# Kernel optimization log

Measured on AMD Instinct MI355X. Metric: run time of the kernel, lower is better.

The kernel has to match this reference:

```python
import jax, jax.numpy as jnp
import numpy as np

H, C = 8, 16          # heads, per-head dim; hidden = H*C = 128
NEG_SLOPE = 0.2       # GATConv default
EPS = 1e-5            # GraphNorm eps


def setup_inputs() -> dict:
    key = jax.random.key(0)
    ks = iter(jax.random.split(key, 64))
    Np, Na, D, E = 100000, 50000, 128, 500000
    s = 1.0 / np.sqrt(D)

    def w(shape, scale=1.0):
        return jax.random.normal(next(ks), shape, jnp.float32) * scale

    inp = {
        'x_paper': w((Np, D)),
        'x_author': w((Na, D)),
        'edge_writes': jnp.stack([
            jax.random.randint(next(ks), (E,), 0, Na),
            jax.random.randint(next(ks), (E,), 0, Np)]).astype(jnp.int32),
        'edge_cites': jnp.stack([
            jax.random.randint(next(ks), (E,), 0, Np),
            jax.random.randint(next(ks), (E,), 0, Np)]).astype(jnp.int32),
        'W_lin_paper': w((D, 128), s), 'b_lin_paper': jnp.zeros((128,), jnp.float32),
        'W_lin_author': w((D, 128), s), 'b_lin_author': jnp.zeros((128,), jnp.float32),
        'Wsrc_writes': w((128, 128), s), 'Wdst_writes': w((128, 128), s),
        'atts_writes': w((H, C), 0.1), 'attd_writes': w((H, C), 0.1),
        'bias_writes': jnp.zeros((128,), jnp.float32),
        'Wsrc_cites': w((128, 128), s), 'Wdst_cites': w((128, 128), s),
        'atts_cites': w((H, C), 0.1), 'attd_cites': w((H, C), 0.1),
        'bias_cites': jnp.zeros((128,), jnp.float32),
        'gnw_paper': jnp.ones((128,), jnp.float32), 'gnb_paper': jnp.zeros((128,), jnp.float32),
        'gnm_paper': jnp.ones((128,), jnp.float32),
        'gnw_author': jnp.ones((128,), jnp.float32), 'gnb_author': jnp.zeros((128,), jnp.float32),
        'gnm_author': jnp.ones((128,), jnp.float32),
        'W2_paper': w((128, 128), s), 'b2_paper': jnp.zeros((128,), jnp.float32),
        'W2_author': w((128, 128), s), 'b2_author': jnp.zeros((128,), jnp.float32),
    }
    return inp


def _gat(src_emb, dst_emb, ei, Wsrc, Wdst, att_s, att_d, bias, n_dst):
    # PyG GATConv, bipartite input, concat=True, add_self_loops=True (eval / no dropout)
    n_self = min(src_emb.shape[0], n_dst)
    loops = jnp.arange(n_self, dtype=ei.dtype)
    src = jnp.concatenate([ei[0], loops])
    dst = jnp.concatenate([ei[1], loops])
    xs = (src_emb @ Wsrc).reshape(-1, H, C)          # [Ns,H,C]
    xd = (dst_emb @ Wdst).reshape(-1, H, C)          # [Nd,H,C]
    a_s = (xs * att_s).sum(-1)                       # [Ns,H]
    a_d = (xd * att_d).sum(-1)                       # [Nd,H]
    e = jax.nn.leaky_relu(a_s[src] + a_d[dst], NEG_SLOPE)   # [E,H]
    m = jax.ops.segment_max(e, dst, num_segments=n_dst)
    m = jnp.where(jnp.isfinite(m), m, 0.0)           # guard empty segments
    p = jnp.exp(e - m[dst])
    denom = jax.ops.segment_sum(p, dst, num_segments=n_dst)
    alpha = p / (denom[dst] + 1e-16)                 # segment softmax over dst
    msg = xs[src] * alpha[:, :, None]                # [E,H,C]
    out = jax.ops.segment_sum(msg, dst, num_segments=n_dst)  # [Nd,H,C]
    return out.reshape(n_dst, H * C) + bias


def _gnorm(x, w, b, ms):
    mu = x.mean(0)
    o = x - ms * mu
    var = (o * o).mean(0)
    return w * o * jax.lax.rsqrt(var + EPS) + b


def reference(x_paper, x_author, edge_writes, edge_cites,
              W_lin_paper, b_lin_paper, W_lin_author, b_lin_author,
              Wsrc_writes, Wdst_writes, atts_writes, attd_writes, bias_writes,
              Wsrc_cites, Wdst_cites, atts_cites, attd_cites, bias_cites,
              gnw_paper, gnb_paper, gnm_paper, gnw_author, gnb_author, gnm_author,
              W2_paper, b2_paper, W2_author, b2_author):
    emb_p = jax.nn.relu(x_paper @ W_lin_paper + b_lin_paper)
    emb_a = jax.nn.relu(x_author @ W_lin_author + b_lin_author)
    Np = emb_p.shape[0]
    out_p = _gat(emb_a, emb_p, edge_writes, Wsrc_writes, Wdst_writes,
                 atts_writes, attd_writes, bias_writes, Np)
    out_p = out_p + _gat(emb_p, emb_p, edge_cites, Wsrc_cites, Wdst_cites,
                         atts_cites, attd_cites, bias_cites, Np)
    out_a = jnp.zeros((emb_a.shape[0], H * C), x_author.dtype)  # no edge type targets author
    out_p = _gnorm(out_p, gnw_paper, gnb_paper, gnm_paper) @ W2_paper + b2_paper
    out_a = _gnorm(out_a, gnw_author, gnb_author, gnm_author) @ W2_author + b2_author
    return (out_p, out_a)
```

## Files before the change

### kernel.cpp

```cpp
#include <hip/hip_runtime.h>
#include <cstdint>
#include <cstddef>

#define H 8
#define DHID 128
#define BM 64
#define LDST 136
#define NEG_SLOPE 0.2f
#define GN_EPS 1e-5f

#define SCAN_T 256
#define SCAN_I 4

typedef __attribute__((ext_vector_type(8))) short short8;
typedef __attribute__((ext_vector_type(4))) float f32x4;

__device__ __forceinline__ void atomAddF(float* p, float v) {
    __hip_atomic_fetch_add(p, v, __ATOMIC_RELAXED, __HIP_MEMORY_SCOPE_AGENT);
}
__device__ __forceinline__ unsigned short f2bf(float f) {
    uint32_t u = __float_as_uint(f);
    uint32_t r = (u + 0x7FFFu + ((u >> 16) & 1u)) >> 16;
    return (unsigned short)r;
}
__device__ __forceinline__ float bflo(uint32_t v) { return __uint_as_float(v << 16); }
__device__ __forceinline__ float bfhi(uint32_t v) { return __uint_as_float(v & 0xFFFF0000u); }

struct PrepHist {
    const float *Wlp, *Wsc, *Wla, *Wsw, *W2p;
    const float *Wdw, *adw, *asc_, *Wdc, *adc_, *asw_;
    unsigned short *WlinP_p, *WsrcP_c, *WlinP_a, *WsrcP_w, *W2P_p, *VscP_p, *VscP_a;
    const float *bw, *bc, *gnb_a, *W2a, *b2a;
    float *bsum, *row_a, *colsum, *colsumsq;
    unsigned short *xs_w_ph, *xs_c_ph;
    float *as_w_ph, *as_c_ph;
    const int *dst_w, *dst_c;
    int *deg;
    int Ew, nself_w, Ec, nself_c, Np, HB0;
};

__global__ void prep_hist(PrepHist a) {
    int b = blockIdx.x, t = threadIdx.x;
    if (b >= a.HB0) {
        int i = (b - a.HB0) * 256 + t;
        int tw = a.Ew + a.nself_w;
        if (i < tw) {
            int d = (i < a.Ew) ? a.dst_w[i] : (i - a.Ew);
            atomicAdd(&a.deg[d], 1);
        } else {
            int j = i - tw;
            if (j < a.Ec + a.nself_c) {
                int d = (j < a.Ec) ? a.dst_c[j] : (j - a.Ec);
                atomicAdd(&a.deg[a.Np + d], 1);
            }
        }
        return;
    }
    if (b == 56) {
        if (t < 128) {
            a.bsum[t] = a.bw[t] + a.bc[t];
            float acc = a.b2a[t];
            for (int k = 0; k < DHID; ++k) acc += a.gnb_a[k] * a.W2a[k * DHID + t];
            a.row_a[t] = acc;
            a.colsum[t] = 0.f;
            a.colsumsq[t] = 0.f;
            a.xs_w_ph[t] = 0;
            a.xs_c_ph[t] = 0;
        } else if (t < 136) a.as_w_ph[t - 128] = -1e30f;
        else if (t < 144) a.as_c_ph[t - 136] = -1e30f;
        return;
    }
    int j = b >> 3;
    int idx = (b & 7) * 256 + t;
    int lane = idx & 63, kk = (idx >> 6) & 3, nt = idx >> 8;
    int col = nt * 16 + (lane & 15);
    int k0 = kk * 32 + ((lane >> 4) << 3);
    if (j < 5) {
        const float* W = j == 0 ? a.Wlp : j == 1 ? a.Wsc : j == 2 ? a.Wla : j == 3 ? a.Wsw : a.W2p;
        unsigned short* out = j == 0 ? a.WlinP_p : j == 1 ? a.WsrcP_c : j == 2 ? a.WlinP_a
                              : j == 3 ? a.WsrcP_w : a.W2P_p;
        for (int i = 0; i < 8; ++i) out[idx * 8 + i] = f2bf(W[(k0 + i) * DHID + col]);
    } else if (j == 5) {
        if (idx >= 2 * 256) return;
        const float *W = nullptr, *A = nullptr;
        int h = col & 7;
        if (col < 24) {
            int which = col >> 3;
            W = which == 0 ? a.Wdw : which == 1 ? a.Wsc : a.Wdc;
            A = which == 0 ? a.adw : which == 1 ? a.asc_ : a.adc_;
        }
        for (int i = 0; i < 8; ++i) {
            float v = 0.f;
            if (W)
                for (int c = 0; c < 16; ++c) v += W[(k0 + i) * DHID + h * 16 + c] * A[h * 16 + c];
            a.VscP_p[idx * 8 + i] = f2bf(v);
        }
    } else {
        if (idx >= 256) return;
        int h = col & 7;
        for (int i = 0; i < 8; ++i) {
            float v = 0.f;
            if (col < 8)
                for (int c = 0; c < 16; ++c)
                    v += a.Wsw[(k0 + i) * DHID + h * 16 + c] * a.asw_[h * 16 + c];
            a.VscP_a[idx * 8 + i] = f2bf(v);
        }
    }
}

__global__ void scan1(const int* __restrict__ in, int n, int* __restrict__ out,
                      int* __restrict__ bsums, int pad, int* __restrict__ totalOut) {
    __shared__ int sh[SCAN_T];
    int t = threadIdx.x;
    long base = (long)blockIdx.x * SCAN_T * SCAN_I;
    int v[SCAN_I];
    int s = 0;
#pragma unroll
    for (int j = 0; j < SCAN_I; ++j) {
        long idx = base + (long)t * SCAN_I + j;
        int x = (idx < n) ? in[idx] : 0;
        if (pad) x = (x + 3) & ~3;
        v[j] = x;
        s += x;
    }
    sh[t] = s;
    __syncthreads();
    for (int off = 1; off < SCAN_T; off <<= 1) {
        int x = (t >= off) ? sh[t - off] : 0;
        __syncthreads();
        sh[t] += x;
        __syncthreads();
    }
    int run = sh[t] - s;
#pragma unroll
    for (int j = 0; j < SCAN_I; ++j) {
        long idx = base + (long)t * SCAN_I + j;
        if (idx < n) out[idx] = run;
        run += v[j];
    }
    if (t == SCAN_T - 1) {
        bsums[blockIdx.x] = sh[SCAN_T - 1];
        if (totalOut) *totalOut = sh[SCAN_T - 1];
    }
}

__global__ void scan3_prefill(const int* __restrict__ off_raw, const int* __restrict__ bs1,
                              int n2, int* __restrict__ off2, int* __restrict__ cur,
                              int Np, int Na, int maxTot, int* __restrict__ srcu) {
    int i = blockIdx.x * 256 + threadIdx.x;
    if (i < n2) {
        int v = off_raw[i] + bs1[i / (SCAN_T * SCAN_I)];
        off2[i] = v;
        cur[i] = v;
    }
    int mid = off_raw[Np] + bs1[Np / (SCAN_T * SCAN_I)];
    long stride = (long)gridDim.x * 256;
    for (long k = i; k < maxTot; k += stride) srcu[k] = (k < (long)mid) ? Na : Np;
}

template <int NSC>
__device__ void proj_body(unsigned short* xt, int bid,
                          const float* __restrict__ x, int nrows,
                          const unsigned short* __restrict__ WlinP, const float* __restrict__ blin,
                          const unsigned short* __restrict__ WsrcP,
                          const unsigned short* __restrict__ VscP,
                          unsigned short* __restrict__ xs,
                          float* __restrict__ a0, float* __restrict__ a1, float* __restrict__ a2) {
    int t = threadIdx.x;
    int lane = t & 63, w = t >> 6;
    long row0 = (long)bid * BM;
    for (int it = 0; it < 16; ++it) {
        int idx2 = t + it * 256;
        int r = idx2 >> 6, cp = idx2 & 63;
        long gr = row0 + r;
        float v0 = 0.f, v1 = 0.f;
        if (gr < nrows) { v0 = x[gr * DHID + 2 * cp]; v1 = x[gr * DHID + 2 * cp + 1]; }
        uint32_t pk = (uint32_t)f2bf(v0) | ((uint32_t)f2bf(v1) << 16);
        *reinterpret_cast<uint32_t*>(&xt[r * LDST + 2 * cp]) = pk;
    }
    __syncthreads();
    int arow = w * 16 + (lane & 15);
    int koff = (lane >> 4) << 3;
    short8 af[4];
#pragma unroll
    for (int kk = 0; kk < 4; ++kk)
        af[kk] = *reinterpret_cast<const short8*>(&xt[arow * LDST + kk * 32 + koff]);
    const short8* Bl = reinterpret_cast<const short8*>(WlinP);
    f32x4 acc[8];
#pragma unroll
    for (int nt = 0; nt < 8; ++nt) {
        f32x4 a = {0.f, 0.f, 0.f, 0.f};
#pragma unroll
        for (int kk = 0; kk < 4; ++kk)
            a = __builtin_amdgcn_mfma_f32_16x16x32_bf16(af[kk], Bl[(nt * 4 + kk) * 64 + lane], a, 0, 0, 0);
        acc[nt] = a;
    }
    __syncthreads();
    int orow = w * 16 + ((lane >> 4) << 2);
    int ccol = lane & 15;
#pragma unroll
    for (int nt = 0; nt < 8; ++nt) {
        float b = blin[nt * 16 + ccol];
#pragma unroll
        for (int r = 0; r < 4; ++r) {
            float e = fmaxf(acc[nt][r] + b, 0.f);
            xt[(orow + r) * LDST + nt * 16 + ccol] = f2bf(e);
        }
    }
    __syncthreads();
#pragma unroll
    for (int kk = 0; kk < 4; ++kk)
        af[kk] = *reinterpret_cast<const short8*>(&xt[arow * LDST + kk * 32 + koff]);
    const short8* Bs = reinterpret_cast<const short8*>(WsrcP);
#pragma unroll
    for (int nt = 0; nt < 8; ++nt) {
        f32x4 a = {0.f, 0.f, 0.f, 0.f};
#pragma unroll
        for (int kk = 0; kk < 4; ++kk)
            a = __builtin_amdgcn_mfma_f32_16x16x32_bf16(af[kk], Bs[(nt * 4 + kk) * 64 + lane], a, 0, 0, 0);
        acc[nt] = a;
    }
    const short8* Bv = reinterpret_cast<const short8*>(VscP);
    f32x4 sacc0 = {0.f, 0.f, 0.f, 0.f}, sacc1 = {0.f, 0.f, 0.f, 0.f};
#pragma unroll
    for (int kk = 0; kk < 4; ++kk)
        sacc0 = __builtin_amdgcn_mfma_f32_16x16x32_bf16(af[kk], Bv[kk * 64 + lane], sacc0, 0, 0, 0);
    if (NSC > 1) {
#pragma unroll
        for (int kk = 0; kk < 4; ++kk)
            sacc1 = __builtin_amdgcn_mfma_f32_16x16x32_bf16(af[kk], Bv[(4 + kk) * 64 + lane], sacc1, 0, 0, 0);
    }
#pragma unroll
    for (int nt = 0; nt < 8; ++nt) {
#pragma unroll
        for (int r = 0; r < 4; ++r) {
            long gr = row0 + orow + r;
            if (gr < nrows) xs[gr * DHID + nt * 16 + ccol] = f2bf(acc[nt][r]);
        }
    }
#pragma unroll
    for (int st = 0; st < NSC; ++st) {
        int scol = st * 16 + ccol;
        int h = scol & 7, which = scol >> 3;
        float* ap = which == 0 ? a0 : which == 1 ? a1 : which == 2 ? a2 : nullptr;
        if (ap) {
            f32x4 s = st == 0 ? sacc0 : sacc1;
#pragma unroll
            for (int r = 0; r < 4; ++r) {
                long gr = row0 + orow + r;
                if (gr < nrows) ap[gr * H + h] = s[r];
            }
        }
    }
}

struct MegaArgs {
    const float* x_p; int Np;
    const unsigned short* WlinP_p; const float* blp;
    const unsigned short* WsrcP_c; const unsigned short* VscP_p;
    unsigned short* xs_c; float *a_d_w, *a_s_c, *a_d_c;
    const float* x_a; int Na;
    const unsigned short* WlinP_a; const float* bla;
    const unsigned short* WsrcP_w; const unsigned short* VscP_a;
    unsigned short* xs_w; float* a_s_w;
    const int *src_w, *dst_w, *src_c, *dst_c;
    int Ew, nself_w, Ec, nself_c;
    int *cur, *srcu;
    int PB, AB;
};

__global__ __launch_bounds__(256) void mega(MegaArgs a) {
    __shared__ unsigned short xt[BM * LDST];
    int b = blockIdx.x;
    if (b < a.PB) {
        proj_body<2>(xt, b, a.x_p, a.Np, a.WlinP_p, a.blp, a.WsrcP_c, a.VscP_p,
                     a.xs_c, a.a_d_w, a.a_s_c, a.a_d_c);
        return;
    }
    if (b < a.PB + a.AB) {
        proj_body<1>(xt, b - a.PB, a.x_a, a.Na, a.WlinP_a, a.bla, a.WsrcP_w, a.VscP_a,
                     a.xs_w, a.a_s_w, nullptr, nullptr);
        return;
    }
    int i = (b - a.PB - a.AB) * 256 + threadIdx.x;
    int tw = a.Ew + a.nself_w;
    int s, di;
    if (i < tw) {
        if (i < a.Ew) { s = a.src_w[i]; di = a.dst_w[i]; } else { s = di = i - a.Ew; }
    } else {
        int j = i - tw;
        if (j >= a.Ec + a.nself_c) return;
        if (j < a.Ec) { s = a.src_c[j]; di = a.Np + a.dst_c[j]; }
        else { s = j - a.Ec; di = a.Np + (j - a.Ec); }
    }
    int pos = atomicAdd(&a.cur[di], 1);
    a.srcu[pos] = s;
}

__global__ __launch_bounds__(256) void gat_gather(
    const int* __restrict__ off, const int* __restrict__ srcu,
    const float* __restrict__ a_s_w, const float* __restrict__ a_d_w,
    const float* __restrict__ a_s_c, const float* __restrict__ a_d_c,
    const unsigned short* __restrict__ xs_w, const unsigned short* __restrict__ xs_c,
    float* __restrict__ gat, int Np) {
    int l = threadIdx.x & 63;
    int d = blockIdx.x * 4 + (threadIdx.x >> 6);
    if (d >= Np) return;
    int h = l >> 3;
    int iw = off[d], w1 = off[d + 1];
    int ic = off[Np + d], c1 = off[Np + d + 1];
    float adw = a_d_w[(long)d * H + h];
    float adc = a_d_c[(long)d * H + h];
    float denw = 0.f, n0w = 0.f, n1w = 0.f;
    float denc = 0.f, n0c = 0.f, n1c = 0.f;
    while (iw < w1 || ic < c1) {
        bool hw = iw < w1, hc = ic < c1;
        int4 sw, sc;
        if (hw) sw = *reinterpret_cast<const int4*>(srcu + iw);
        if (hc) sc = *reinterpret_cast<const int4*>(srcu + ic);
        float ew[4], ec[4];
        uint32_t vw[4], vc[4];
        if (hw) {
            ew[0] = a_s_w[(long)sw.x * H + h];
            ew[1] = a_s_w[(long)sw.y * H + h];
            ew[2] = a_s_w[(long)sw.z * H + h];
            ew[3] = a_s_w[(long)sw.w * H + h];
            vw[0] = *reinterpret_cast<const uint32_t*>(xs_w + (long)sw.x * DHID + 2 * l);
            vw[1] = *reinterpret_cast<const uint32_t*>(xs_w + (long)sw.y * DHID + 2 * l);
            vw[2] = *reinterpret_cast<const uint32_t*>(xs_w + (long)sw.z * DHID + 2 * l);
            vw[3] = *reinterpret_cast<const uint32_t*>(xs_w + (long)sw.w * DHID + 2 * l);
        }
        if (hc) {
            ec[0] = a_s_c[(long)sc.x * H + h];
            ec[1] = a_s_c[(long)sc.y * H + h];
            ec[2] = a_s_c[(long)sc.z * H + h];
            ec[3] = a_s_c[(long)sc.w * H + h];
            vc[0] = *reinterpret_cast<const uint32_t*>(xs_c + (long)sc.x * DHID + 2 * l);
            vc[1] = *reinterpret_cast<const uint32_t*>(xs_c + (long)sc.y * DHID + 2 * l);
            vc[2] = *reinterpret_cast<const uint32_t*>(xs_c + (long)sc.z * DHID + 2 * l);
            vc[3] = *reinterpret_cast<const uint32_t*>(xs_c + (long)sc.w * DHID + 2 * l);
        }
        if (hw) {
#pragma unroll
            for (int j = 0; j < 4; ++j) {
                float e = ew[j] + adw;
                e = e > 0.f ? e : NEG_SLOPE * e;
                float p = __expf(e);
                denw += p;
                n0w += p * bflo(vw[j]);
                n1w += p * bfhi(vw[j]);
            }
            iw += 4;
        }
        if (hc) {
#pragma unroll
            for (int j = 0; j < 4; ++j) {
                float e = ec[j] + adc;
                e = e > 0.f ? e : NEG_SLOPE * e;
                float p = __expf(e);
                denc += p;
                n0c += p * bflo(vc[j]);
                n1c += p * bfhi(vc[j]);
            }
            ic += 4;
        }
    }
    float rw = 1.f / (denw + 1e-16f);
    float rc = 1.f / (denc + 1e-16f);
    float2 o;
    o.x = n0w * rw + n0c * rc;
    o.y = n1w * rw + n1c * rc;
    *reinterpret_cast<float2*>(&gat[(long)d * DHID + 2 * l]) = o;
}

#define GN_ROWS 128
__global__ void gn_reduce(const float* __restrict__ gat, const float* __restrict__ bsum,
                          float* __restrict__ colsum, float* __restrict__ colsumsq, int Np) {
    int t = threadIdx.x;
    long r0 = (long)blockIdx.x * GN_ROWS;
    long r1 = min(r0 + GN_ROWS, (long)Np);
    float b = bsum[t], s1 = 0.f, s2 = 0.f;
    for (long r = r0; r < r1; ++r) {
        float xv = gat[r * DHID + t] + b;
        s1 += xv;
        s2 += xv * xv;
    }
    atomAddF(colsum + t, s1);
    atomAddF(colsumsq + t, s2);
}

__global__ __launch_bounds__(256) void final_fill(
    const float* __restrict__ gat, const float* __restrict__ bsum,
    const float* __restrict__ colsum, const float* __restrict__ colsumsq,
    const float* __restrict__ gnw, const float* __restrict__ gnb,
    const float* __restrict__ gnm,
    const unsigned short* __restrict__ W2P, const float* __restrict__ b2,
    float* __restrict__ out, int Np, int FB,
    const float* __restrict__ row_a, float4* __restrict__ outa, long n4) {
    __shared__ unsigned short xt[BM * LDST];
    __shared__ float cscale[DHID], cshift[DHID];
    int b = blockIdx.x;
    int t = threadIdx.x;
    if (b >= FB) {
        long i = (long)(b - FB) * 256 + t;
        long stride = (long)(gridDim.x - FB) * 256;
        const float4* r4 = reinterpret_cast<const float4*>(row_a);
        for (; i < n4; i += stride) outa[i] = r4[i & 31];
        return;
    }
    int lane = t & 63, w = t >> 6;
    long row0 = (long)b * BM;
    if (t < DHID) {
        float invN = 1.f / (float)Np;
        float mu = colsum[t] * invN;
        float ms = gnm[t];
        float var = colsumsq[t] * invN - mu * mu * ms * (2.f - ms);
        float sc = gnw[t] * rsqrtf(var + GN_EPS);
        cscale[t] = sc;
        cshift[t] = (bsum[t] - ms * mu) * sc + gnb[t];
    }
    __syncthreads();
    for (int it = 0; it < 16; ++it) {
        int idx2 = t + it * 256;
        int r = idx2 >> 6, cp = idx2 & 63;
        long gr = row0 + r;
        float v0 = 0.f, v1 = 0.f;
        if (gr < Np) {
            v0 = gat[gr * DHID + 2 * cp] * cscale[2 * cp] + cshift[2 * cp];
            v1 = gat[gr * DHID + 2 * cp + 1] * cscale[2 * cp + 1] + cshift[2 * cp + 1];
        }
        uint32_t pk = (uint32_t)f2bf(v0) | ((uint32_t)f2bf(v1) << 16);
        *reinterpret_cast<uint32_t*>(&xt[r * LDST + 2 * cp]) = pk;
    }
    __syncthreads();
    int arow = w * 16 + (lane & 15);
    int koff = (lane >> 4) << 3;
    short8 af[4];
#pragma unroll
    for (int kk = 0; kk < 4; ++kk)
        af[kk] = *reinterpret_cast<const short8*>(&xt[arow * LDST + kk * 32 + koff]);
    const short8* Bw = reinterpret_cast<const short8*>(W2P);
    int orow = w * 16 + ((lane >> 4) << 2);
    int ccol = lane & 15;
#pragma unroll
    for (int nt = 0; nt < 8; ++nt) {
        f32x4 a = {0.f, 0.f, 0.f, 0.f};
#pragma unroll
        for (int kk = 0; kk < 4; ++kk)
            a = __builtin_amdgcn_mfma_f32_16x16x32_bf16(af[kk], Bw[(nt * 4 + kk) * 64 + lane], a, 0, 0, 0);
        float bb = b2[nt * 16 + ccol];
#pragma unroll
        for (int r = 0; r < 4; ++r) {
            long gr = row0 + orow + r;
            if (gr < Np) out[gr * DHID + nt * 16 + ccol] = a[r] + bb;
        }
    }
}

extern "C" void kernel_launch(void* const* d_in, const int* in_sizes, int n_in,
                              void* d_out, int out_size, void* d_ws, size_t ws_size,
                              hipStream_t stream) {
    const float* x_p   = (const float*)d_in[0];
    const float* x_a   = (const float*)d_in[1];
    const int*   e_w   = (const int*)d_in[2];
    const int*   e_c   = (const int*)d_in[3];
    const float* Wlp   = (const float*)d_in[4];
    const float* blp   = (const float*)d_in[5];
    const float* Wla   = (const float*)d_in[6];
    const float* bla   = (const float*)d_in[7];
    const float* Wsw   = (const float*)d_in[8];
    const float* Wdw   = (const float*)d_in[9];
    const float* asw   = (const float*)d_in[10];
    const float* adw   = (const float*)d_in[11];
    const float* bw    = (const float*)d_in[12];
    const float* Wsc   = (const float*)d_in[13];
    const float* Wdc   = (const float*)d_in[14];
    const float* asc   = (const float*)d_in[15];
    const float* adc   = (const float*)d_in[16];
    const float* bc    = (const float*)d_in[17];
    const float* gnw_p = (const float*)d_in[18];
    const float* gnb_p = (const float*)d_in[19];
    const float* gnm_p = (const float*)d_in[20];
    const float* gnb_a = (const float*)d_in[22];
    const float* W2p   = (const float*)d_in[24];
    const float* b2p   = (const float*)d_in[25];
    const float* W2a   = (const float*)d_in[26];
    const float* b2a   = (const float*)d_in[27];

    int Np = in_sizes[0] / DHID;
    int Na = in_sizes[1] / DHID;
    int Ew = in_sizes[2] / 2;
    int Ec = in_sizes[3] / 2;
    int nself_w = Na < Np ? Na : Np;
    int nself_c = Np;
    int tot_all = (Ew + nself_w) + (Ec + nself_c);
    int maxTot = tot_all + 6 * Np + 8;

    float* ws = (float*)d_ws;
    float* gat   = ws;
    float* a_d_w = gat + (size_t)Np * DHID;
    float* a_d_c = a_d_w + (size_t)Np * H;
    float* a_s_w = a_d_c + (size_t)Np * H;
    float* a_s_c = a_s_w + (size_t)(Na + 1) * H;
    float* bsum  = a_s_c + (size_t)(Np + 1) * H;
    float* row_a = bsum + DHID;
    float* colsum   = row_a + DHID;
    float* colsumsq = colsum + DHID;
    int*   deg   = (int*)(colsumsq + DHID);
    int* off_raw = deg + 2 * Np;
    int* off2    = off_raw + 2 * Np;
    int* cur     = off2 + 2 * Np + 1;
    int* bs1     = cur + 2 * Np;
    int* bs2     = bs1 + 512;
    uintptr_t up = (uintptr_t)(bs2 + 512);
    up = (up + 15) & ~(uintptr_t)15;
    int* srcu = (int*)up;
    unsigned short* xs_w = (unsigned short*)(srcu + maxTot);
    unsigned short* xs_c = xs_w + (size_t)(Na + 1) * DHID;
    up = (uintptr_t)(xs_c + (size_t)(Np + 1) * DHID);
    up = (up + 15) & ~(uintptr_t)15;
    unsigned short* WlinP_p = (unsigned short*)up;
    unsigned short* WsrcP_c = WlinP_p + 16384;
    unsigned short* WlinP_a = WsrcP_c + 16384;
    unsigned short* WsrcP_w = WlinP_a + 16384;
    unsigned short* W2P_p   = WsrcP_w + 16384;
    unsigned short* VscP_p  = W2P_p + 16384;
    unsigned short* VscP_a  = VscP_p + 4096;

    hipMemsetAsync(deg, 0, 2 * (size_t)Np * sizeof(int), stream);

    int HB = (tot_all + 255) / 256;
    {
        PrepHist pa;
        pa.Wlp = Wlp; pa.Wsc = Wsc; pa.Wla = Wla; pa.Wsw = Wsw; pa.W2p = W2p;
        pa.Wdw = Wdw; pa.adw = adw; pa.asc_ = asc; pa.Wdc = Wdc; pa.adc_ = adc; pa.asw_ = asw;
        pa.WlinP_p = WlinP_p; pa.WsrcP_c = WsrcP_c; pa.WlinP_a = WlinP_a;
        pa.WsrcP_w = WsrcP_w; pa.W2P_p = W2P_p; pa.VscP_p = VscP_p; pa.VscP_a = VscP_a;
        pa.bw = bw; pa.bc = bc; pa.gnb_a = gnb_a; pa.W2a = W2a; pa.b2a = b2a;
        pa.bsum = bsum; pa.row_a = row_a; pa.colsum = colsum; pa.colsumsq = colsumsq;
        pa.xs_w_ph = xs_w + (size_t)Na * DHID;
        pa.xs_c_ph = xs_c + (size_t)Np * DHID;
        pa.as_w_ph = a_s_w + (size_t)Na * H;
        pa.as_c_ph = a_s_c + (size_t)Np * H;
        pa.dst_w = e_w + Ew; pa.dst_c = e_c + Ec;
        pa.deg = deg;
        pa.Ew = Ew; pa.nself_w = nself_w; pa.Ec = Ec; pa.nself_c = nself_c;
        pa.Np = Np; pa.HB0 = 57;
        prep_hist<<<57 + HB, 256, 0, stream>>>(pa);
    }

    int n2 = 2 * Np;
    int nb = (n2 + SCAN_T * SCAN_I - 1) / (SCAN_T * SCAN_I);
    scan1<<<nb, SCAN_T, 0, stream>>>(deg, n2, off_raw, bs1, 1, nullptr);
    scan1<<<1, SCAN_T, 0, stream>>>(bs1, nb, bs1, bs2, 0, off2 + n2);

    scan3_prefill<<<(maxTot + 255) / 256, 256, 0, stream>>>(
        off_raw, bs1, n2, off2, cur, Np, Na, maxTot, srcu);

    {
        MegaArgs ma;
        ma.x_p = x_p; ma.Np = Np; ma.WlinP_p = WlinP_p; ma.blp = blp;
        ma.WsrcP_c = WsrcP_c; ma.VscP_p = VscP_p;
        ma.xs_c = xs_c; ma.a_d_w = a_d_w; ma.a_s_c = a_s_c; ma.a_d_c = a_d_c;
        ma.x_a = x_a; ma.Na = Na; ma.WlinP_a = WlinP_a; ma.bla = bla;
        ma.WsrcP_w = WsrcP_w; ma.VscP_a = VscP_a;
        ma.xs_w = xs_w; ma.a_s_w = a_s_w;
        ma.src_w = e_w; ma.dst_w = e_w + Ew; ma.src_c = e_c; ma.dst_c = e_c + Ec;
        ma.Ew = Ew; ma.nself_w = nself_w; ma.Ec = Ec; ma.nself_c = nself_c;
        ma.cur = cur; ma.srcu = srcu;
        ma.PB = (Np + BM - 1) / BM;
        ma.AB = (Na + BM - 1) / BM;
        int SB = (tot_all + 255) / 256;
        mega<<<ma.PB + ma.AB + SB, 256, 0, stream>>>(ma);
    }

    gat_gather<<<(Np + 3) / 4, 256, 0, stream>>>(off2, srcu,
                                                 a_s_w, a_d_w, a_s_c, a_d_c,
                                                 xs_w, xs_c, gat, Np);

    gn_reduce<<<(Np + GN_ROWS - 1) / GN_ROWS, 128, 0, stream>>>(gat, bsum, colsum, colsumsq, Np);

    {
        int FB = (Np + BM - 1) / BM;
        long n4 = (long)Na * DHID / 4;
        final_fill<<<FB + 391, 256, 0, stream>>>(
            gat, bsum, colsum, colsumsq, gnw_p, gnb_p, gnm_p, W2P_p, b2p,
            (float*)d_out, Np, FB,
            row_a, (float4*)((float*)d_out + (size_t)Np * DHID), n4);
    }
}
```

Before: 308.3 us.

## Record per-edge rank in histogram pass and interleave projection with scatter blocks

The histogram kernel now stores the atomic return value as each edge's rank within its destination bucket. The CSR scatter can then write to off2[dst]+rank directly, with no second round of atomics and no cur array to initialise. Projection blocks and scatter blocks in the mega kernel are also spread evenly across the grid instead of being placed back to back, so the two kinds of work can run concurrently. The cost is an extra rank array that is written in one pass and read back in the other.

```diff
diff --git a/kernel.cpp b/kernel.cpp
--- a/kernel.cpp
+++ b/kernel.cpp
@@ -35,7 +35,7 @@
     unsigned short *xs_w_ph, *xs_c_ph;
     float *as_w_ph, *as_c_ph;
     const int *dst_w, *dst_c;
-    int *deg;
+    int *deg, *rank;
     int Ew, nself_w, Ec, nself_c, Np, HB0;
 };
 
@@ -46,12 +46,12 @@
         int tw = a.Ew + a.nself_w;
         if (i < tw) {
             int d = (i < a.Ew) ? a.dst_w[i] : (i - a.Ew);
-            atomicAdd(&a.deg[d], 1);
+            a.rank[i] = atomicAdd(&a.deg[d], 1);
         } else {
             int j = i - tw;
             if (j < a.Ec + a.nself_c) {
                 int d = (j < a.Ec) ? a.dst_c[j] : (j - a.Ec);
-                atomicAdd(&a.deg[a.Np + d], 1);
+                a.rank[i] = atomicAdd(&a.deg[a.Np + d], 1);
             }
         }
         return;
@@ -145,14 +145,10 @@
 }
 
 __global__ void scan3_prefill(const int* __restrict__ off_raw, const int* __restrict__ bs1,
-                              int n2, int* __restrict__ off2, int* __restrict__ cur,
+                              int n2, int* __restrict__ off2,
                               int Np, int Na, int maxTot, int* __restrict__ srcu) {
     int i = blockIdx.x * 256 + threadIdx.x;
-    if (i < n2) {
-        int v = off_raw[i] + bs1[i / (SCAN_T * SCAN_I)];
-        off2[i] = v;
-        cur[i] = v;
-    }
+    if (i < n2) off2[i] = off_raw[i] + bs1[i / (SCAN_T * SCAN_I)];
     int mid = off_raw[Np] + bs1[Np / (SCAN_T * SCAN_I)];
     long stride = (long)gridDim.x * 256;
     for (long k = i; k < maxTot; k += stride) srcu[k] = (k < (long)mid) ? Na : Np;
@@ -265,24 +261,30 @@
     unsigned short* xs_w; float* a_s_w;
     const int *src_w, *dst_w, *src_c, *dst_c;
     int Ew, nself_w, Ec, nself_c;
-    int *cur, *srcu;
+    const int *off2, *rank;
+    int* srcu;
     int PB, AB;
 };
 
 __global__ __launch_bounds__(256) void mega(MegaArgs a) {
     __shared__ unsigned short xt[BM * LDST];
     int b = blockIdx.x;
-    if (b < a.PB) {
-        proj_body<2>(xt, b, a.x_p, a.Np, a.WlinP_p, a.blp, a.WsrcP_c, a.VscP_p,
-                     a.xs_c, a.a_d_w, a.a_s_c, a.a_d_c);
+    int G = gridDim.x;
+    int nP = a.PB + a.AB;
+    long fb  = (long)b * nP / G;
+    long fb1 = (long)(b + 1) * nP / G;
+    if (fb1 > fb) {
+        int pb = (int)fb;
+        if (pb < a.PB)
+            proj_body<2>(xt, pb, a.x_p, a.Np, a.WlinP_p, a.blp, a.WsrcP_c, a.VscP_p,
+                         a.xs_c, a.a_d_w, a.a_s_c, a.a_d_c);
+        else
+            proj_body<1>(xt, pb - a.PB, a.x_a, a.Na, a.WlinP_a, a.bla, a.WsrcP_w, a.VscP_a,
+                         a.xs_w, a.a_s_w, nullptr, nullptr);
         return;
     }
-    if (b < a.PB + a.AB) {
-        proj_body<1>(xt, b - a.PB, a.x_a, a.Na, a.WlinP_a, a.bla, a.WsrcP_w, a.VscP_a,
-                     a.xs_w, a.a_s_w, nullptr, nullptr);
-        return;
-    }
-    int i = (b - a.PB - a.AB) * 256 + threadIdx.x;
+    int sb = b - (int)fb;
+    int i = sb * 256 + threadIdx.x;
     int tw = a.Ew + a.nself_w;
     int s, di;
     if (i < tw) {
@@ -293,8 +295,7 @@
         if (j < a.Ec) { s = a.src_c[j]; di = a.Np + a.dst_c[j]; }
         else { s = j - a.Ec; di = a.Np + (j - a.Ec); }
     }
-    int pos = atomicAdd(&a.cur[di], 1);
-    a.srcu[pos] = s;
+    a.srcu[a.off2[di] + a.rank[i]] = s;
 }
 
 __global__ __launch_bounds__(256) void gat_gather(
@@ -509,13 +510,13 @@
     int*   deg   = (int*)(colsumsq + DHID);
     int* off_raw = deg + 2 * Np;
     int* off2    = off_raw + 2 * Np;
-    int* cur     = off2 + 2 * Np + 1;
-    int* bs1     = cur + 2 * Np;
+    int* bs1     = off2 + 2 * Np + 1;
     int* bs2     = bs1 + 512;
     uintptr_t up = (uintptr_t)(bs2 + 512);
     up = (up + 15) & ~(uintptr_t)15;
     int* srcu = (int*)up;
-    unsigned short* xs_w = (unsigned short*)(srcu + maxTot);
+    int* rank = srcu + maxTot;
+    unsigned short* xs_w = (unsigned short*)(rank + tot_all);
     unsigned short* xs_c = xs_w + (size_t)(Na + 1) * DHID;
     up = (uintptr_t)(xs_c + (size_t)(Np + 1) * DHID);
     up = (up + 15) & ~(uintptr_t)15;
@@ -543,7 +544,7 @@
         pa.as_w_ph = a_s_w + (size_t)Na * H;
         pa.as_c_ph = a_s_c + (size_t)Np * H;
         pa.dst_w = e_w + Ew; pa.dst_c = e_c + Ec;
-        pa.deg = deg;
+        pa.deg = deg; pa.rank = rank;
         pa.Ew = Ew; pa.nself_w = nself_w; pa.Ec = Ec; pa.nself_c = nself_c;
         pa.Np = Np; pa.HB0 = 57;
         prep_hist<<<57 + HB, 256, 0, stream>>>(pa);
@@ -555,7 +556,7 @@
     scan1<<<1, SCAN_T, 0, stream>>>(bs1, nb, bs1, bs2, 0, off2 + n2);
 
     scan3_prefill<<<(maxTot + 255) / 256, 256, 0, stream>>>(
-        off_raw, bs1, n2, off2, cur, Np, Na, maxTot, srcu);
+        off_raw, bs1, n2, off2, Np, Na, maxTot, srcu);
 
     {
         MegaArgs ma;
@@ -567,7 +568,7 @@
         ma.xs_w = xs_w; ma.a_s_w = a_s_w;
         ma.src_w = e_w; ma.dst_w = e_w + Ew; ma.src_c = e_c; ma.dst_c = e_c + Ec;
         ma.Ew = Ew; ma.nself_w = nself_w; ma.Ec = Ec; ma.nself_c = nself_c;
-        ma.cur = cur; ma.srcu = srcu;
+        ma.off2 = off2; ma.rank = rank; ma.srcu = srcu;
         ma.PB = (Np + BM - 1) / BM;
         ma.AB = (Na + BM - 1) / BM;
         int SB = (tot_all + 255) / 256;
```

Measured after the change: 311.0 us. No clear change (+0.9%).
